# Optimization experiments

Hardware: AMD Instinct MI355X
Metric: run time of the kernel (lower is better)

The kernel has to match this reference:

```python
import jax, jax.numpy as jnp
import numpy as np

B, F, E = 2048, 200, 64

def setup_inputs() -> dict:
    key = jax.random.key(0)
    k1, k2 = jax.random.split(key)
    feature = jax.random.normal(k1, (B, F, E), dtype=jnp.float32)
    # nn.init.normal(weight, mean=0, std=0.01)
    weight = 0.01 * jax.random.normal(k2, (F, E, E), dtype=jnp.float32)
    return {"feature": feature, "weight": weight}

def reference(feature, weight):
    # biLinear[b,i,d] = sum_e feature[b,i,e] * weight[i,e,d]   (per-feature bilinear projection)
    bilinear = jnp.einsum('bie,ied->bid', feature, weight)
    # out[b,i,j] = sum_d bilinear[b,i,d] * feature[b,j,d]      (pairwise dot, avoids (B,F,F,E) temp)
    out = jnp.einsum('bid,bjd->bij', bilinear, feature)
    return out
```

## Files before the change

### kernel.cpp

```cpp
#include <hip/hip_runtime.h>


typedef short bx8  __attribute__((ext_vector_type(8)));
typedef float f32x4 __attribute__((ext_vector_type(4)));

constexpr int Bb = 2048, Ff = 200, Ee = 64;

__device__ __forceinline__ ushort bf16h(float x) {
    uint u = __float_as_uint(x);
    return (ushort)((u + 0x7FFFu + ((u >> 16) & 1u)) >> 16);
}
__device__ __forceinline__ float bf16f(ushort h) {
    return __uint_as_float(((uint)h) << 16);
}

__global__ __launch_bounds__(256, 3)
void k1_bilinear(const float* __restrict__ feat, const float* __restrict__ wgt,
                 uint* __restrict__ bilP) {
    __shared__ ushort fH[128 * 64], fL[128 * 64];
    __shared__ ushort wH[64 * 64],  wL[64 * 64];
    const int i  = blockIdx.y;
    const int b0 = blockIdx.x << 7;
    const int t  = threadIdx.x;

    for (int q = t; q < 2048; q += 256) {
        const int row = q >> 4, e0 = (q & 15) << 2;
        const float4 v = *reinterpret_cast<const float4*>(
            feat + ((size_t)(b0 + row) * Ff + i) * Ee + e0);
        const float vv[4] = {v.x, v.y, v.z, v.w};
        ushort hh[4], ll[4];
#pragma unroll
        for (int j = 0; j < 4; ++j) {
            hh[j] = bf16h(vv[j]);
            ll[j] = bf16h(vv[j] - bf16f(hh[j]));
        }
        const int idx = row * 64 + (e0 ^ ((row & 7) << 3));
        *reinterpret_cast<ushort4*>(&fH[idx]) = make_ushort4(hh[0], hh[1], hh[2], hh[3]);
        *reinterpret_cast<ushort4*>(&fL[idx]) = make_ushort4(ll[0], ll[1], ll[2], ll[3]);
    }
    for (int q = t; q < 2048; q += 256) {
        const int e = (q >> 6) << 1;
        const int d = q & 63;
        const float x0 = wgt[((size_t)i * Ee + e) * Ee + d];
        const float x1 = wgt[((size_t)i * Ee + e + 1) * Ee + d];
        const ushort h0 = bf16h(x0), h1 = bf16h(x1);
        const ushort l0 = bf16h(x0 - bf16f(h0)), l1 = bf16h(x1 - bf16f(h1));
        const int idx = d * 64 + (e ^ ((d & 7) << 3));
        *reinterpret_cast<uint*>(&wH[idx]) = (uint)h0 | ((uint)h1 << 16);
        *reinterpret_cast<uint*>(&wL[idx]) = (uint)l0 | ((uint)l1 << 16);
    }
    __syncthreads();

    const int lane = t & 63, w = t >> 6;
    const int r16 = lane & 15, g = lane >> 4;
    f32x4 acc[2][4];
#pragma unroll
    for (int a = 0; a < 2; ++a)
#pragma unroll
        for (int j = 0; j < 4; ++j) acc[a][j] = (f32x4){0.f, 0.f, 0.f, 0.f};

#pragma unroll
    for (int ks = 0; ks < 2; ++ks) {
        const int coff = ks * 32 + (g << 3);
        bx8 AH[2], AL[2];
#pragma unroll
        for (int it = 0; it < 2; ++it) {
            const int row = (w * 2 + it) * 16 + r16;
            const int idx = row * 64 + (coff ^ ((row & 7) << 3));
            AH[it] = *reinterpret_cast<const bx8*>(&fH[idx]);
            AL[it] = *reinterpret_cast<const bx8*>(&fL[idx]);
        }
#pragma unroll
        for (int jt = 0; jt < 4; ++jt) {
            const int col = jt * 16 + r16;
            const int idx = col * 64 + (coff ^ ((col & 7) << 3));
            const bx8 BH = *reinterpret_cast<const bx8*>(&wH[idx]);
            const bx8 BL = *reinterpret_cast<const bx8*>(&wL[idx]);
#pragma unroll
            for (int it = 0; it < 2; ++it) {
                acc[it][jt] = __builtin_amdgcn_mfma_f32_16x16x32_bf16(AH[it], BH, acc[it][jt], 0, 0, 0);
                acc[it][jt] = __builtin_amdgcn_mfma_f32_16x16x32_bf16(AH[it], BL, acc[it][jt], 0, 0, 0);
                acc[it][jt] = __builtin_amdgcn_mfma_f32_16x16x32_bf16(AL[it], BH, acc[it][jt], 0, 0, 0);
            }
        }
    }
#pragma unroll
    for (int it = 0; it < 2; ++it) {
#pragma unroll
        for (int jt = 0; jt < 4; ++jt) {
            const int d = jt * 16 + r16;
#pragma unroll
            for (int reg = 0; reg < 4; ++reg) {
                const int brow = b0 + (w * 2 + it) * 16 + (g << 2) + reg;
                const float x = acc[it][jt][reg];
                const ushort h = bf16h(x);
                const ushort l = bf16h(x - bf16f(h));
                bilP[((size_t)brow * Ff + i) * Ee + d] = (uint)h | ((uint)l << 16);
            }
        }
    }
}

__global__ __launch_bounds__(512, 4)
void k2_outer(const float* __restrict__ feat, const uint* __restrict__ bilP,
              float* __restrict__ out) {
    __shared__ ushort fjH[208 * 32], fjL[208 * 32];
    __shared__ ushort aH[112 * 32],  aL[112 * 32];
    const int ihalf = blockIdx.x, b = blockIdx.y;
    const int t = threadIdx.x;
    const int lane = t & 63, w = t >> 6;
    const int r16 = lane & 15, g = lane >> 4;
    const int nstrips = ihalf ? 6 : 7;
    const int i0base = ihalf * 112;

    f32x4 acc[13];
#pragma unroll
    for (int jt = 0; jt < 13; ++jt) acc[jt] = (f32x4){0.f, 0.f, 0.f, 0.f};

#pragma unroll
    for (int ks = 0; ks < 2; ++ks) {
        for (int q = t; q < 1664; q += 512) {
            const int j = q >> 3, c0 = (q & 7) << 2;
            float4 v = {0.f, 0.f, 0.f, 0.f};
            if (j < Ff)
                v = *reinterpret_cast<const float4*>(
                    feat + ((size_t)b * Ff + j) * Ee + ks * 32 + c0);
            const float vv[4] = {v.x, v.y, v.z, v.w};
            ushort hh[4], ll[4];
#pragma unroll
            for (int u = 0; u < 4; ++u) {
                hh[u] = bf16h(vv[u]);
                ll[u] = bf16h(vv[u] - bf16f(hh[u]));
            }
            const int idx = j * 32 + (c0 ^ ((j & 3) << 3));
            *reinterpret_cast<ushort4*>(&fjH[idx]) = make_ushort4(hh[0], hh[1], hh[2], hh[3]);
            *reinterpret_cast<ushort4*>(&fjL[idx]) = make_ushort4(ll[0], ll[1], ll[2], ll[3]);
        }
        for (int q = t; q < 896; q += 512) {
            const int r = q >> 3, c0 = (q & 7) << 2;
            const int gi = i0base + r;
            uint4 v = {0u, 0u, 0u, 0u};
            if (gi < Ff)
                v = *reinterpret_cast<const uint4*>(
                    bilP + ((size_t)b * Ff + gi) * Ee + ks * 32 + c0);
            const uint vv[4] = {v.x, v.y, v.z, v.w};
            const int idx = r * 32 + (c0 ^ ((r & 3) << 3));
            *reinterpret_cast<ushort4*>(&aH[idx]) = make_ushort4(
                (ushort)(vv[0] & 0xFFFF), (ushort)(vv[1] & 0xFFFF),
                (ushort)(vv[2] & 0xFFFF), (ushort)(vv[3] & 0xFFFF));
            *reinterpret_cast<ushort4*>(&aL[idx]) = make_ushort4(
                (ushort)(vv[0] >> 16), (ushort)(vv[1] >> 16),
                (ushort)(vv[2] >> 16), (ushort)(vv[3] >> 16));
        }
        __syncthreads();

        if (w < nstrips) {
            const int arow = w * 16 + r16;
            const int cof = g << 3;
            const int aidx = arow * 32 + (cof ^ ((arow & 3) << 3));
            const bx8 AH = *reinterpret_cast<const bx8*>(&aH[aidx]);
            const bx8 AL = *reinterpret_cast<const bx8*>(&aL[aidx]);
#pragma unroll
            for (int jt = 0; jt < 13; ++jt) {
                const int jrow = jt * 16 + r16;
                const int bidx = jrow * 32 + (cof ^ ((jrow & 3) << 3));
                const bx8 BH = *reinterpret_cast<const bx8*>(&fjH[bidx]);
                const bx8 BL = *reinterpret_cast<const bx8*>(&fjL[bidx]);
                acc[jt] = __builtin_amdgcn_mfma_f32_16x16x32_bf16(AH, BH, acc[jt], 0, 0, 0);
                acc[jt] = __builtin_amdgcn_mfma_f32_16x16x32_bf16(AH, BL, acc[jt], 0, 0, 0);
                acc[jt] = __builtin_amdgcn_mfma_f32_16x16x32_bf16(AL, BH, acc[jt], 0, 0, 0);
            }
        }
        __syncthreads();
    }

    if (w < nstrips) {
        const int ibase = i0base + w * 16 + (g << 2);
#pragma unroll
        for (int jt = 0; jt < 13; ++jt) {
            const int col = jt * 16 + r16;
            if (col < Ff) {
#pragma unroll
                for (int reg = 0; reg < 4; ++reg) {
                    const int irow = ibase + reg;
                    if (irow < Ff)
                        out[((size_t)b * Ff + irow) * Ff + col] = acc[jt][reg];
                }
            }
        }
    }
}

extern "C" void kernel_launch(void* const* d_in, const int* in_sizes, int n_in,
                              void* d_out, int out_size, void* d_ws, size_t ws_size,
                              hipStream_t stream) {
    const float* feat = (const float*)d_in[0];
    const float* wgt  = (const float*)d_in[1];
    float* out = (float*)d_out;
    uint* bilP = (uint*)d_ws;

    k1_bilinear<<<dim3(Bb / 128, Ff), 256, 0, stream>>>(feat, wgt, bilP);
    k2_outer<<<dim3(2, Bb), 512, 0, stream>>>(feat, bilP, out);
}
```

Before: 535.0 us.

## Process all output rows per batch in one block, loading A fragments directly from global

The second kernel now launches one block per batch instead of two half-blocks. Each block converts the full 200x64 feature tile to hi/lo bf16 in shared memory once, so the two i-halves no longer both convert it. The bilinear A operand is read straight from global memory into registers, which removes its shared staging and the per-k-step barriers. The cost is half as many blocks, larger shared memory per block (about 53 KB), and uneven work across the 8 waves: 13 strips split so 5 waves do two strips. That may lower occupancy and leave some waves idle.

```diff
diff --git a/kernel.cpp b/kernel.cpp
--- a/kernel.cpp
+++ b/kernel.cpp
@@ -104,66 +104,58 @@
 __global__ __launch_bounds__(512, 4)
 void k2_outer(const float* __restrict__ feat, const uint* __restrict__ bilP,
               float* __restrict__ out) {
-    __shared__ ushort fjH[208 * 32], fjL[208 * 32];
-    __shared__ ushort aH[112 * 32],  aL[112 * 32];
-    const int ihalf = blockIdx.x, b = blockIdx.y;
+    __shared__ ushort fjH[208 * 64], fjL[208 * 64];
+    const int b = blockIdx.x;
     const int t = threadIdx.x;
     const int lane = t & 63, w = t >> 6;
     const int r16 = lane & 15, g = lane >> 4;
-    const int nstrips = ihalf ? 6 : 7;
-    const int i0base = ihalf * 112;
 
-    f32x4 acc[13];
+    for (int q = t; q < 3328; q += 512) {
+        const int j = q >> 4, c0 = (q & 15) << 2;
+        float4 v = {0.f, 0.f, 0.f, 0.f};
+        if (j < Ff)
+            v = *reinterpret_cast<const float4*>(feat + ((size_t)b * Ff + j) * Ee + c0);
+        const float vv[4] = {v.x, v.y, v.z, v.w};
+        ushort hh[4], ll[4];
 #pragma unroll
-    for (int jt = 0; jt < 13; ++jt) acc[jt] = (f32x4){0.f, 0.f, 0.f, 0.f};
+        for (int u = 0; u < 4; ++u) {
+            hh[u] = bf16h(vv[u]);
+            ll[u] = bf16h(vv[u] - bf16f(hh[u]));
+        }
+        const int idx = j * 64 + (c0 ^ ((j & 7) << 3));
+        *reinterpret_cast<ushort4*>(&fjH[idx]) = make_ushort4(hh[0], hh[1], hh[2], hh[3]);
+        *reinterpret_cast<ushort4*>(&fjL[idx]) = make_ushort4(ll[0], ll[1], ll[2], ll[3]);
+    }
+    __syncthreads();
 
 #pragma unroll
-    for (int ks = 0; ks < 2; ++ks) {
-        for (int q = t; q < 1664; q += 512) {
-            const int j = q >> 3, c0 = (q & 7) << 2;
-            float4 v = {0.f, 0.f, 0.f, 0.f};
-            if (j < Ff)
-                v = *reinterpret_cast<const float4*>(
-                    feat + ((size_t)b * Ff + j) * Ee + ks * 32 + c0);
-            const float vv[4] = {v.x, v.y, v.z, v.w};
-            ushort hh[4], ll[4];
+    for (int si = 0; si < 2; ++si) {
+        const int strip = w + si * 8;
+        if (strip > 12) break;
+        const int i0 = strip * 16;
+        const int arow = (i0 + r16 < Ff) ? (i0 + r16) : (Ff - 1);
+
+        f32x4 acc[13];
 #pragma unroll
-            for (int u = 0; u < 4; ++u) {
-                hh[u] = bf16h(vv[u]);
-                ll[u] = bf16h(vv[u] - bf16f(hh[u]));
+        for (int jt = 0; jt < 13; ++jt) acc[jt] = (f32x4){0.f, 0.f, 0.f, 0.f};
+
+#pragma unroll
+        for (int kp = 0; kp < 2; ++kp) {
+            const uint* src = bilP + ((size_t)b * Ff + arow) * Ee + kp * 32 + g * 8;
+            const uint4 v0 = *reinterpret_cast<const uint4*>(src);
+            const uint4 v1 = *reinterpret_cast<const uint4*>(src + 4);
+            const uint vv[8] = {v0.x, v0.y, v0.z, v0.w, v1.x, v1.y, v1.z, v1.w};
+            bx8 AH, AL;
+#pragma unroll
+            for (int u = 0; u < 8; ++u) {
+                AH[u] = (short)(vv[u] & 0xFFFFu);
+                AL[u] = (short)(vv[u] >> 16);
             }
-            const int idx = j * 32 + (c0 ^ ((j & 3) << 3));
-            *reinterpret_cast<ushort4*>(&fjH[idx]) = make_ushort4(hh[0], hh[1], hh[2], hh[3]);
-            *reinterpret_cast<ushort4*>(&fjL[idx]) = make_ushort4(ll[0], ll[1], ll[2], ll[3]);
-        }
-        for (int q = t; q < 896; q += 512) {
-            const int r = q >> 3, c0 = (q & 7) << 2;
-            const int gi = i0base + r;
-            uint4 v = {0u, 0u, 0u, 0u};
-            if (gi < Ff)
-                v = *reinterpret_cast<const uint4*>(
-                    bilP + ((size_t)b * Ff + gi) * Ee + ks * 32 + c0);
-            const uint vv[4] = {v.x, v.y, v.z, v.w};
-            const int idx = r * 32 + (c0 ^ ((r & 3) << 3));
-            *reinterpret_cast<ushort4*>(&aH[idx]) = make_ushort4(
-                (ushort)(vv[0] & 0xFFFF), (ushort)(vv[1] & 0xFFFF),
-                (ushort)(vv[2] & 0xFFFF), (ushort)(vv[3] & 0xFFFF));
-            *reinterpret_cast<ushort4*>(&aL[idx]) = make_ushort4(
-                (ushort)(vv[0] >> 16), (ushort)(vv[1] >> 16),
-                (ushort)(vv[2] >> 16), (ushort)(vv[3] >> 16));
-        }
-        __syncthreads();
-
-        if (w < nstrips) {
-            const int arow = w * 16 + r16;
-            const int cof = g << 3;
-            const int aidx = arow * 32 + (cof ^ ((arow & 3) << 3));
-            const bx8 AH = *reinterpret_cast<const bx8*>(&aH[aidx]);
-            const bx8 AL = *reinterpret_cast<const bx8*>(&aL[aidx]);
+            const int c = kp * 32 + (g << 3);
 #pragma unroll
             for (int jt = 0; jt < 13; ++jt) {
                 const int jrow = jt * 16 + r16;
-                const int bidx = jrow * 32 + (cof ^ ((jrow & 3) << 3));
+                const int bidx = jrow * 64 + (c ^ ((jrow & 7) << 3));
                 const bx8 BH = *reinterpret_cast<const bx8*>(&fjH[bidx]);
                 const bx8 BL = *reinterpret_cast<const bx8*>(&fjL[bidx]);
                 acc[jt] = __builtin_amdgcn_mfma_f32_16x16x32_bf16(AH, BH, acc[jt], 0, 0, 0);
@@ -171,11 +163,8 @@
                 acc[jt] = __builtin_amdgcn_mfma_f32_16x16x32_bf16(AL, BH, acc[jt], 0, 0, 0);
             }
         }
-        __syncthreads();
-    }
 
-    if (w < nstrips) {
-        const int ibase = i0base + w * 16 + (g << 2);
+        const int ibase = i0 + (g << 2);
 #pragma unroll
         for (int jt = 0; jt < 13; ++jt) {
             const int col = jt * 16 + r16;
@@ -200,5 +189,5 @@
     uint* bilP = (uint*)d_ws;
 
     k1_bilinear<<<dim3(Bb / 128, Ff), 256, 0, stream>>>(feat, wgt, bilP);
-    k2_outer<<<dim3(2, Bb), 512, 0, stream>>>(feat, bilP, out);
+    k2_outer<<<Bb, 512, 0, stream>>>(feat, bilP, out);
 }
```

After: 504.6 us. -5.7%, faster.
